# Optimization experiments

Hardware: AMD Instinct MI355X
Metric: run time of the kernel (lower is better)

## Reference

```python
import jax, jax.numpy as jnp
import numpy as np

DIM = 256
HEADS = 8
DIM_HEAD = 64
EPS = 1e-12  # F.normalize eps


def rms_norm(x, w, dim):
    # F.normalize over channel dim (axis=1) * weight * sqrt(dim)
    n = jnp.sqrt(jnp.sum(x * x, axis=1, keepdims=True))
    xn = x / jnp.maximum(n, EPS)
    return xn * w[None, :, None, None] * (dim ** 0.5)


def setup_inputs() -> dict:
    key = jax.random.key(0)
    ks = jax.random.split(key, 4)
    hd = HEADS * DIM_HEAD
    return {
        "x": jax.random.normal(ks[0], (16, DIM, 64, 64), dtype=jnp.float32),
        "norm_w": jnp.ones((DIM,), jnp.float32),
        "qkv_w": jax.random.normal(ks[1], (3 * hd, DIM), jnp.float32) * (DIM ** -0.5),
        "out_w": jax.random.normal(ks[2], (DIM, hd), jnp.float32) * (hd ** -0.5),
        "out_b": jnp.zeros((DIM,), jnp.float32),
        "out_norm_w": jnp.ones((DIM,), jnp.float32),
    }


def reference(x, norm_w, qkv_w, out_w, out_b, out_norm_w):
    b, c, H, W = x.shape
    n = H * W
    scale = DIM_HEAD ** -0.5

    xn = rms_norm(x, norm_w, DIM)
    # 1x1 conv == channel matmul: [3hd, c] x [b, c, H, W]
    qkv = jnp.einsum('oc,bchw->bohw', qkv_w, xn)
    q, k, v = jnp.split(qkv, 3, axis=1)

    def to_heads(t):
        # b (h d) x y -> b h d n
        return t.reshape(b, HEADS, DIM_HEAD, n)

    q = jax.nn.softmax(to_heads(q), axis=2) * scale  # softmax over feature dim d
    k = jax.nn.softmax(to_heads(k), axis=3)          # softmax over spatial n
    v = to_heads(v)

    ctx = jnp.einsum('bhdn,bhen->bhde', k, v)   # [b,h,d,e]
    out = jnp.einsum('bhde,bhdn->bhen', ctx, q) # [b,h,e,n]
    out = out.reshape(b, HEADS * DIM_HEAD, H, W)

    out = jnp.einsum('oc,bchw->bohw', out_w, out) + out_b[None, :, None, None]
    return rms_norm(out, out_norm_w, DIM)
```

## Files before the change

kernel.cpp:

```cpp
#include <hip/hip_runtime.h>

#define C_ 256
#define N_ 4096
#define NH_ 8

typedef unsigned short u16;
typedef unsigned int u32;
typedef __attribute__((ext_vector_type(8))) short s8v;
typedef __attribute__((ext_vector_type(4))) float f4v;

#define MFMA16 __builtin_amdgcn_mfma_f32_16x16x32_bf16

__device__ __forceinline__ float bf2f(u16 b){ union{u32 u; float f;} v; v.u=((u32)b)<<16; return v.f; }
__device__ __forceinline__ u16 f2bf(float f){ union{float f; u32 u;} v; v.f=f; return (u16)((v.u + 0x7FFFu + ((v.u>>16)&1u))>>16); }

__device__ __forceinline__ void gl_lds16(const u16* g, u16* l){
  __builtin_amdgcn_global_load_lds((const __attribute__((address_space(1))) u32*)g,
                                   (__attribute__((address_space(3))) u32*)l, 16, 0, 0);
}

__global__ __launch_bounds__(256) void k_prep(const float* __restrict__ x, const float* __restrict__ nw,
                                              u16* __restrict__ xnT){
  __shared__ float red[256];
  __shared__ float nws[256];
  const int tid = threadIdx.x;
  nws[tid] = nw[tid];
  const int blk = blockIdx.x, b = blk>>6, n0 = (blk&63)*64;
  const int cq = tid>>6, px = tid&63;
  const float* xp = x + (size_t)b*(C_*N_) + (size_t)(cq*64)*N_ + n0 + px;
  float v[64]; float s = 0.f;
  #pragma unroll
  for (int i=0;i<64;i++){ float t = xp[(size_t)i*N_]; v[i]=t; s = fmaf(t,t,s); }
  red[tid] = s;
  __syncthreads();
  const float st = red[px] + red[64+px] + red[128+px] + red[192+px];
  const float r = 16.0f / fmaxf(sqrtf(st), 1e-12f);
  u16* o = xnT + ((size_t)b*4096 + n0 + px)*256 + cq*64;
  #pragma unroll
  for (int i=0;i<64;i+=2){
    *(u32*)(o+i) = (u32)f2bf(v[i]*r*nws[cq*64+i]) | ((u32)f2bf(v[i+1]*r*nws[cq*64+i+1])<<16);
  }
}

__global__ __launch_bounds__(256) void k_wconv(const float* __restrict__ qkvw, const float* __restrict__ ow,
                                               u16* __restrict__ wqkv, u16* __restrict__ owb){
  int i = blockIdx.x*256 + threadIdx.x;
  if (i < 393216) wqkv[i] = f2bf(qkvw[i]);
  else            owb[i-393216] = f2bf(ow[i-393216]);
}

__global__ __launch_bounds__(256,3) void k_kv(const u16* __restrict__ xnT, const u16* __restrict__ wqkv,
    u16* __restrict__ ctxp, float* __restrict__ Mp, float* __restrict__ Sp){
  __shared__ u16 xs[64*256];
  __shared__ u16 pbuf[64*72];
  __shared__ u16 vbuf[64*72];
  const int idx = blockIdx.x;
  const int ch = idx&7, h = (idx>>3)&7, b = idx>>6;
  const int tid=threadIdx.x, w=tid>>6, l=tid&63, l15=l&15, lg=l>>4;
  const int swl = (l15&7)<<4;
  const u16* xb  = xnT + (size_t)b*(4096*256);
  const int srow = (l>>5);
  const int scolB = (l&31)*16;
  s8v ak[8], av[8];
  {
    const u16* wkp = wqkv + (size_t)(512 + h*64 + w*16 + l15)*256 + lg*8;
    #pragma unroll
    for (int cs=0; cs<8; cs++){ ak[cs] = *(const s8v*)(wkp + cs*32); av[cs] = *(const s8v*)(wkp + 131072 + cs*32); }
  }
  int colOff[8];
  #pragma unroll
  for (int cs=0; cs<8; cs++) colOff[cs] = (((cs<<6)+(lg<<4)) ^ swl)>>1;

  f4v acc[4];
  #pragma unroll
  for (int et=0;et<4;et++) acc[et] = (f4v){0.f,0.f,0.f,0.f};
  float ps[4] = {0.f,0.f,0.f,0.f};

  {
    const int n0 = ch*512;
    #pragma unroll
    for (int i=0;i<8;i++){
      int rloc = w*16 + i*2 + srow;
      int scol = scolB ^ ((rloc&7)<<4);
      gl_lds16(xb + (size_t)(n0+rloc)*256 + (scol>>1), &xs[(w*16+i*2)*256]);
    }
  }

  for (int t=0; t<8; ++t){
    __syncthreads();
    f4v kacc[4], vacc[4];
    #pragma unroll
    for (int ns=0;ns<4;ns++){ kacc[ns]=(f4v){0.f,0.f,0.f,0.f}; vacc[ns]=(f4v){0.f,0.f,0.f,0.f}; }
    #pragma unroll
    for (int cs=0; cs<8; cs++){
      #pragma unroll
      for (int ns=0; ns<4; ns++){
        s8v bfr = *(const s8v*)&xs[(ns*16+l15)*256 + colOff[cs]];
        kacc[ns] = MFMA16(ak[cs], bfr, kacc[ns], 0,0,0);
        vacc[ns] = MFMA16(av[cs], bfr, vacc[ns], 0,0,0);
      }
    }
    #pragma unroll
    for (int j=0;j<4;j++){
      const int row = w*16 + lg*4 + j;
      #pragma unroll
      for (int ns=0;ns<4;ns++){
        float e = __expf(kacc[ns][j] - 30.0f);
        ps[j] += e;
        pbuf[row*72 + ns*16+l15] = f2bf(e);
        vbuf[row*72 + ns*16+l15] = f2bf(vacc[ns][j]);
      }
    }
    __syncthreads();
    if (t<7){
      const int n0 = ch*512 + (t+1)*64;
      #pragma unroll
      for (int i=0;i<8;i++){
        int rloc = w*16 + i*2 + srow;
        int scol = scolB ^ ((rloc&7)<<4);
        gl_lds16(xb + (size_t)(n0+rloc)*256 + (scol>>1), &xs[(w*16+i*2)*256]);
      }
    }
    #pragma unroll
    for (int ks=0; ks<2; ks++){
      s8v af = *(const s8v*)(pbuf + (w*16+l15)*72 + ks*32 + lg*8);
      #pragma unroll
      for (int et=0; et<4; et++){
        s8v bv = *(const s8v*)(vbuf + (et*16+l15)*72 + ks*32 + lg*8);
        acc[et] = MFMA16(af, bv, acc[et], 0,0,0);
      }
    }
  }
  u16* cp = ctxp + (((size_t)ch*16 + b)*8 + h)*4096;
  #pragma unroll
  for (int et=0; et<4; et++)
    #pragma unroll
    for (int j=0;j<4;j++)
      cp[(w*16+lg*4+j)*64 + et*16+l15] = f2bf(acc[et][j]);
  #pragma unroll
  for (int j=0;j<4;j++){
    float s = ps[j];
    s += __shfl_xor(s,1); s += __shfl_xor(s,2);
    s += __shfl_xor(s,4); s += __shfl_xor(s,8);
    ps[j] = s;
  }
  if (l15==0){
    #pragma unroll
    for (int j=0;j<4;j++){
      int rg = (b*8+h)*64 + w*16 + lg*4 + j;
      Mp[ch*8192+rg]=30.0f; Sp[ch*8192+rg]=ps[j];
    }
  }
}

__global__ __launch_bounds__(256) void k_comb(const u16* __restrict__ ctxp, const float* __restrict__ Mp,
    const float* __restrict__ Sp, u16* __restrict__ ctxT){
  __shared__ float fs[8][64];
  __shared__ float iSs[64];
  const int bh = blockIdx.x, tid = threadIdx.x;
  if (tid < 64){
    float m[8];
    float Mg = -1e30f;
    #pragma unroll
    for (int ch=0;ch<8;ch++){ m[ch] = Mp[ch*8192 + bh*64 + tid]; Mg = fmaxf(Mg, m[ch]); }
    float Sg = 0.f;
    #pragma unroll
    for (int ch=0;ch<8;ch++){
      float fv = __expf(m[ch]-Mg);
      fs[ch][tid] = fv;
      Sg += Sp[ch*8192 + bh*64 + tid]*fv;
    }
    iSs[tid] = 1.0f / Sg;
  }
  __syncthreads();
  const int e = tid>>2, d0 = (tid&3)*16;
  u16* op = ctxT + (size_t)bh*4096 + e*64 + d0;
  #pragma unroll
  for (int i=0;i<16;i++){
    int d = d0+i;
    float v = 0.f;
    #pragma unroll
    for (int ch=0;ch<8;ch++)
      v += bf2f(ctxp[((size_t)(ch*128)+bh)*4096 + d*64 + e]) * fs[ch][d];
    op[i] = f2bf(v * iSs[d]);
  }
}

__global__ __launch_bounds__(512,2) void k_qout(const u16* __restrict__ xnT, const u16* __restrict__ wqkv,
    const u16* __restrict__ owb, const u16* __restrict__ ctxT,
    const float* __restrict__ ob, const float* __restrict__ onw, float* __restrict__ out){
  __shared__ u16 WQb[2][64*256];
  __shared__ u16 OWb[2][256*64];
  __shared__ u16 qa[8][16*72];
  __shared__ float obs[256], onws[256];
  const int tid = threadIdx.x;
  if (tid < 256){ obs[tid]=ob[tid]; onws[tid]=onw[tid]; }
  const int w=tid>>6, l=tid&63, l15=l&15, lg=l>>4;
  const int swl = (l15&7)<<4;
  const int blk=blockIdx.x, b=blk>>5, n0=(blk&31)*128 + w*16;
  const u16* xb = xnT + ((size_t)b*4096 + n0)*256;
  const u16* cxb0 = ctxT + ((size_t)b*8)*4096;
  u16* qaw = qa[w];
  const int wqRowB = w*8 + (l>>5);
  const int wqColB = (l&31)*16;
  const int owRowB = w*32 + (l>>3);
  const int owColB = (l&7)*16;
  s8v ax[8];
  #pragma unroll
  for (int cs=0;cs<8;cs++) ax[cs] = *(const s8v*)(xb + (size_t)l15*256 + cs*32 + lg*8);
  f4v oacc[16];
  #pragma unroll
  for (int mt=0;mt<16;mt++) oacc[mt] = (f4v){0.f,0.f,0.f,0.f};

  {
    const u16* wqg = wqkv;
    #pragma unroll
    for (int i=0;i<4;i++){
      int row = wqRowB + i*2;
      int scol = wqColB ^ ((row&7)<<4);
      gl_lds16(wqg + (size_t)row*256 + (scol>>1), &WQb[0][(w*8+i*2)*256]);
    }
    #pragma unroll
    for (int i=0;i<4;i++){
      int row = owRowB + i*8;
      int scol = owColB ^ ((row&7)<<4);
      gl_lds16(owb + (size_t)row*512 + 0 + (scol>>1), &OWb[0][(w*32+i*8)*64]);
    }
  }

  for (int h=0; h<8; ++h){
    const int p = h&1;
    asm volatile("s_waitcnt vmcnt(0)" ::: "memory");
    __builtin_amdgcn_s_barrier();
    __builtin_amdgcn_sched_barrier(0);
    s8v bc[8];
    {
      const u16* cxb = cxb0 + (size_t)h*4096;
      #pragma unroll
      for (int ks=0; ks<2; ks++)
        #pragma unroll
        for (int et=0; et<4; et++)
          bc[ks*4+et] = *(const s8v*)(cxb + (et*16+l15)*64 + ks*32 + lg*8);
    }
    if (h<7){
      const u16* wqg = wqkv + (size_t)(h+1)*64*256;
      #pragma unroll
      for (int i=0;i<4;i++){
        int row = wqRowB + i*2;
        int scol = wqColB ^ ((row&7)<<4);
        gl_lds16(wqg + (size_t)row*256 + (scol>>1), &WQb[p^1][(w*8+i*2)*256]);
      }
      #pragma unroll
      for (int i=0;i<4;i++){
        int row = owRowB + i*8;
        int scol = owColB ^ ((row&7)<<4);
        gl_lds16(owb + (size_t)row*512 + (h+1)*64 + (scol>>1), &OWb[p^1][(w*32+i*8)*64]);
      }
    }
    f4v qacc[4];
    #pragma unroll
    for (int dt=0;dt<4;dt++) qacc[dt] = (f4v){0.f,0.f,0.f,0.f};
    #pragma unroll
    for (int dt=0; dt<4; dt++){
      #pragma unroll
      for (int cs=0; cs<8; cs++){
        s8v bw = *(const s8v*)&WQb[p][(dt*16+l15)*256 + ((((cs<<6)+(lg<<4)) ^ swl)>>1)];
        qacc[dt] = MFMA16(ax[cs], bw, qacc[dt], 0,0,0);
      }
    }
    #pragma unroll
    for (int j=0;j<4;j++){
      float m = fmaxf(fmaxf(qacc[0][j],qacc[1][j]),fmaxf(qacc[2][j],qacc[3][j]));
      #pragma unroll
      for (int d=1; d<16; d<<=1) m = fmaxf(m, __shfl_xor(m, d));
      float s = 0.f;
      #pragma unroll
      for (int dt=0;dt<4;dt++){ float e=__expf(qacc[dt][j]-m); qacc[dt][j]=e; s+=e; }
      #pragma unroll
      for (int d=1; d<16; d<<=1) s += __shfl_xor(s, d);
      float inv = 0.125f/s;
      #pragma unroll
      for (int dt=0;dt<4;dt++) qaw[(lg*4+j)*72 + dt*16+l15] = f2bf(qacc[dt][j]*inv);
    }
    f4v aacc[4];
    #pragma unroll
    for (int et=0;et<4;et++) aacc[et] = (f4v){0.f,0.f,0.f,0.f};
    #pragma unroll
    for (int ks=0; ks<2; ks++){
      s8v aq = *(const s8v*)&qaw[l15*72 + ks*32 + lg*8];
      #pragma unroll
      for (int et=0; et<4; et++)
        aacc[et] = MFMA16(aq, bc[ks*4+et], aacc[et], 0,0,0);
    }
    #pragma unroll
    for (int et=0;et<4;et++)
      #pragma unroll
      for (int j=0;j<4;j++)
        qaw[(lg*4+j)*72 + et*16+l15] = f2bf(aacc[et][j]);
    #pragma unroll
    for (int ks=0; ks<2; ks++){
      s8v ba = *(const s8v*)&qaw[l15*72 + ks*32 + lg*8];
      #pragma unroll
      for (int mt=0; mt<16; mt++){
        s8v aw = *(const s8v*)&OWb[p][(mt*16+l15)*64 + ((((ks<<6)+(lg<<4)) ^ swl)>>1)];
        oacc[mt] = MFMA16(aw, ba, oacc[mt], 0,0,0);
      }
    }
  }
  float ss = 0.f;
  #pragma unroll
  for (int mt=0;mt<16;mt++)
    #pragma unroll
    for (int j=0;j<4;j++){
      float v = oacc[mt][j] + obs[mt*16+lg*4+j];
      oacc[mt][j] = v;
      ss = fmaf(v,v,ss);
    }
  ss += __shfl_xor(ss, 16);
  ss += __shfl_xor(ss, 32);
  const float r = 16.0f / fmaxf(sqrtf(ss), 1e-12f);
  float* op = out + (size_t)b*(256*4096) + n0 + l15;
  #pragma unroll
  for (int mt=0;mt<16;mt++)
    #pragma unroll
    for (int j=0;j<4;j++){
      int cout = mt*16+lg*4+j;
      op[(size_t)cout*4096] = oacc[mt][j] * r * onws[cout];
    }
}

extern "C" void kernel_launch(void* const* d_in, const int* in_sizes, int n_in,
                              void* d_out, int out_size, void* d_ws, size_t ws_size,
                              hipStream_t stream){
  const float* x    = (const float*)d_in[0];
  const float* nw   = (const float*)d_in[1];
  const float* qkvw = (const float*)d_in[2];
  const float* ow   = (const float*)d_in[3];
  const float* ob   = (const float*)d_in[4];
  const float* onw  = (const float*)d_in[5];
  float* out = (float*)d_out;
  char* ws = (char*)d_ws;
  u16*   xnT  = (u16*)(ws);
  u16*   wqkv = (u16*)(ws + 33554432);
  u16*   owb  = (u16*)(ws + 34340864);
  u16*   ctxT = (u16*)(ws + 34603008);
  u16*   ctxp = (u16*)(ws + 35651584);
  float* Mp   = (float*)(ws + 44040192);
  float* Sp   = (float*)(ws + 44302336);
  (void)in_sizes; (void)n_in; (void)out_size; (void)ws_size;

  k_wconv<<<2048, 256, 0, stream>>>(qkvw, ow, wqkv, owb);
  k_prep <<<1024, 256, 0, stream>>>(x, nw, xnT);
  k_kv   <<<1024, 256, 0, stream>>>(xnT, wqkv, ctxp, Mp, Sp);
  k_comb <<<128, 256, 0, stream>>>(ctxp, Mp, Sp, ctxT);
  k_qout <<<512, 512, 0, stream>>>(xnT, wqkv, owb, ctxT, ob, onw, out);
}
```

Before: 173.7 us.

## Single-buffer LDS weights in k_qout to raise occupancy to four blocks per CU

The double-buffered LDS tiles for the Q and output-projection weight slices become single buffers, and the per-warp q scratch uses a compact XOR-swizzled layout with no padding. This cuts LDS per block so launch bounds can request four blocks per CU instead of two. To keep single buffers correct, the next head's output weights are loaded after the barrier and the next Q weights after a second mid-iteration barrier. Bias and norm weights are read straight from global memory as float4 instead of being staged in LDS. The cost is an extra barrier per head and less overlap between weight loads and compute, and the higher occupancy target squeezes the register budget, which may cause spills.

```diff
diff --git a/kernel.cpp b/kernel.cpp
--- a/kernel.cpp
+++ b/kernel.cpp
@@ -186,24 +186,21 @@
   }
 }
 
-__global__ __launch_bounds__(512,2) void k_qout(const u16* __restrict__ xnT, const u16* __restrict__ wqkv,
+__global__ __launch_bounds__(512,4) void k_qout(const u16* __restrict__ xnT, const u16* __restrict__ wqkv,
     const u16* __restrict__ owb, const u16* __restrict__ ctxT,
     const float* __restrict__ ob, const float* __restrict__ onw, float* __restrict__ out){
-  __shared__ u16 WQb[2][64*256];
-  __shared__ u16 OWb[2][256*64];
-  __shared__ u16 qa[8][16*72];
-  __shared__ float obs[256], onws[256];
+  __shared__ u16 WQ[64*256];
+  __shared__ u16 OWs[256*64];
+  __shared__ u16 qa[8][1024];
   const int tid = threadIdx.x;
-  if (tid < 256){ obs[tid]=ob[tid]; onws[tid]=onw[tid]; }
   const int w=tid>>6, l=tid&63, l15=l&15, lg=l>>4;
-  const int swl = (l15&7)<<4;
   const int blk=blockIdx.x, b=blk>>5, n0=(blk&31)*128 + w*16;
   const u16* xb = xnT + ((size_t)b*4096 + n0)*256;
   const u16* cxb0 = ctxT + ((size_t)b*8)*4096;
   u16* qaw = qa[w];
-  const int wqRowB = w*8 + (l>>5);
+  const int wqRow0 = (l>>5);
   const int wqColB = (l&31)*16;
-  const int owRowB = w*32 + (l>>3);
+  const int owRow0 = (l>>3);
   const int owColB = (l&7)*16;
   s8v ax[8];
   #pragma unroll
@@ -212,24 +209,20 @@
   #pragma unroll
   for (int mt=0;mt<16;mt++) oacc[mt] = (f4v){0.f,0.f,0.f,0.f};
 
-  {
-    const u16* wqg = wqkv;
-    #pragma unroll
-    for (int i=0;i<4;i++){
-      int row = wqRowB + i*2;
-      int scol = wqColB ^ ((row&7)<<4);
-      gl_lds16(wqg + (size_t)row*256 + (scol>>1), &WQb[0][(w*8+i*2)*256]);
-    }
-    #pragma unroll
-    for (int i=0;i<4;i++){
-      int row = owRowB + i*8;
-      int scol = owColB ^ ((row&7)<<4);
-      gl_lds16(owb + (size_t)row*512 + 0 + (scol>>1), &OWb[0][(w*32+i*8)*64]);
-    }
+  #pragma unroll
+  for (int i=0;i<4;i++){
+    int row = (i*8+w)*2 + wqRow0;
+    int scol = wqColB ^ ((row&15)<<4);
+    gl_lds16(wqkv + (size_t)row*256 + (scol>>1), &WQ[(i*8+w)*512]);
+  }
+  #pragma unroll
+  for (int i=0;i<4;i++){
+    int row = (i*8+w)*8 + owRow0;
+    int scol = owColB ^ ((row&7)<<4);
+    gl_lds16(owb + (size_t)row*512 + (scol>>1), &OWs[(i*8+w)*512]);
   }
 
   for (int h=0; h<8; ++h){
-    const int p = h&1;
     asm volatile("s_waitcnt vmcnt(0)" ::: "memory");
     __builtin_amdgcn_s_barrier();
     __builtin_amdgcn_sched_barrier(0);
@@ -242,91 +235,107 @@
         for (int et=0; et<4; et++)
           bc[ks*4+et] = *(const s8v*)(cxb + (et*16+l15)*64 + ks*32 + lg*8);
     }
+    if (h>0){
+      #pragma unroll
+      for (int i=0;i<4;i++){
+        int row = (i*8+w)*8 + owRow0;
+        int scol = owColB ^ ((row&7)<<4);
+        gl_lds16(owb + (size_t)row*512 + h*64 + (scol>>1), &OWs[(i*8+w)*512]);
+      }
+    }
+    __builtin_amdgcn_sched_barrier(0);
+    f4v qacc[4];
+    #pragma unroll
+    for (int dt=0;dt<4;dt++) qacc[dt] = (f4v){0.f,0.f,0.f,0.f};
+    #pragma unroll
+    for (int dt=0; dt<4; dt++){
+      #pragma unroll
+      for (int cs=0; cs<8; cs++){
+        s8v bw = *(const s8v*)&WQ[(dt*16+l15)*256 + ((((cs<<6)|(lg<<4)) ^ (l15<<4))>>1)];
+        qacc[dt] = MFMA16(ax[cs], bw, qacc[dt], 0,0,0);
+      }
+    }
+    #pragma unroll
+    for (int j=0;j<4;j++){
+      float m = fmaxf(fmaxf(qacc[0][j],qacc[1][j]),fmaxf(qacc[2][j],qacc[3][j]));
+      #pragma unroll
+      for (int d=1; d<16; d<<=1) m = fmaxf(m, __shfl_xor(m, d));
+      float s = 0.f;
+      #pragma unroll
+      for (int dt=0;dt<4;dt++){ float e=__expf(qacc[dt][j]-m); qacc[dt][j]=e; s+=e; }
+      #pragma unroll
+      for (int d=1; d<16; d<<=1) s += __shfl_xor(s, d);
+      float inv = 0.125f/s;
+      #pragma unroll
+      for (int dt=0;dt<4;dt++){
+        int row = lg*4+j;
+        qaw[((row<<6) + dt*16 + l15) ^ ((row&7)<<3)] = f2bf(qacc[dt][j]*inv);
+      }
+    }
+    f4v aacc[4];
+    #pragma unroll
+    for (int et=0;et<4;et++) aacc[et] = (f4v){0.f,0.f,0.f,0.f};
+    #pragma unroll
+    for (int ks=0; ks<2; ks++){
+      s8v aq = *(const s8v*)&qaw[(l15<<6) + ((((ks<<6)|(lg<<4)) ^ ((l15&7)<<4))>>1)];
+      #pragma unroll
+      for (int et=0; et<4; et++)
+        aacc[et] = MFMA16(aq, bc[ks*4+et], aacc[et], 0,0,0);
+    }
+    #pragma unroll
+    for (int et=0;et<4;et++)
+      #pragma unroll
+      for (int j=0;j<4;j++){
+        int row = lg*4+j;
+        qaw[((row<<6) + et*16 + l15) ^ ((row&7)<<3)] = f2bf(aacc[et][j]);
+      }
+    asm volatile("s_waitcnt vmcnt(0)" ::: "memory");
+    __builtin_amdgcn_s_barrier();
+    __builtin_amdgcn_sched_barrier(0);
     if (h<7){
       const u16* wqg = wqkv + (size_t)(h+1)*64*256;
       #pragma unroll
       for (int i=0;i<4;i++){
-        int row = wqRowB + i*2;
-        int scol = wqColB ^ ((row&7)<<4);
-        gl_lds16(wqg + (size_t)row*256 + (scol>>1), &WQb[p^1][(w*8+i*2)*256]);
-      }
-      #pragma unroll
-      for (int i=0;i<4;i++){
-        int row = owRowB + i*8;
-        int scol = owColB ^ ((row&7)<<4);
-        gl_lds16(owb + (size_t)row*512 + (h+1)*64 + (scol>>1), &OWb[p^1][(w*32+i*8)*64]);
-      }
-    }
-    f4v qacc[4];
-    #pragma unroll
-    for (int dt=0;dt<4;dt++) qacc[dt] = (f4v){0.f,0.f,0.f,0.f};
-    #pragma unroll
-    for (int dt=0; dt<4; dt++){
-      #pragma unroll
-      for (int cs=0; cs<8; cs++){
-        s8v bw = *(const s8v*)&WQb[p][(dt*16+l15)*256 + ((((cs<<6)+(lg<<4)) ^ swl)>>1)];
-        qacc[dt] = MFMA16(ax[cs], bw, qacc[dt], 0,0,0);
-      }
-    }
-    #pragma unroll
-    for (int j=0;j<4;j++){
-      float m = fmaxf(fmaxf(qacc[0][j],qacc[1][j]),fmaxf(qacc[2][j],qacc[3][j]));
-      #pragma unroll
-      for (int d=1; d<16; d<<=1) m = fmaxf(m, __shfl_xor(m, d));
-      float s = 0.f;
-      #pragma unroll
-      for (int dt=0;dt<4;dt++){ float e=__expf(qacc[dt][j]-m); qacc[dt][j]=e; s+=e; }
-      #pragma unroll
-      for (int d=1; d<16; d<<=1) s += __shfl_xor(s, d);
-      float inv = 0.125f/s;
-      #pragma unroll
-      for (int dt=0;dt<4;dt++) qaw[(lg*4+j)*72 + dt*16+l15] = f2bf(qacc[dt][j]*inv);
-    }
-    f4v aacc[4];
-    #pragma unroll
-    for (int et=0;et<4;et++) aacc[et] = (f4v){0.f,0.f,0.f,0.f};
+        int row = (i*8+w)*2 + wqRow0;
+        int scol = wqColB ^ ((row&15)<<4);
+        gl_lds16(wqg + (size_t)row*256 + (scol>>1), &WQ[(i*8+w)*512]);
+      }
+    }
+    __builtin_amdgcn_sched_barrier(0);
     #pragma unroll
     for (int ks=0; ks<2; ks++){
-      s8v aq = *(const s8v*)&qaw[l15*72 + ks*32 + lg*8];
-      #pragma unroll
-      for (int et=0; et<4; et++)
-        aacc[et] = MFMA16(aq, bc[ks*4+et], aacc[et], 0,0,0);
-    }
-    #pragma unroll
-    for (int et=0;et<4;et++)
-      #pragma unroll
-      for (int j=0;j<4;j++)
-        qaw[(lg*4+j)*72 + et*16+l15] = f2bf(aacc[et][j]);
-    #pragma unroll
-    for (int ks=0; ks<2; ks++){
-      s8v ba = *(const s8v*)&qaw[l15*72 + ks*32 + lg*8];
+      s8v ba = *(const s8v*)&qaw[(l15<<6) + ((((ks<<6)|(lg<<4)) ^ ((l15&7)<<4))>>1)];
       #pragma unroll
       for (int mt=0; mt<16; mt++){
-        s8v aw = *(const s8v*)&OWb[p][(mt*16+l15)*64 + ((((ks<<6)+(lg<<4)) ^ swl)>>1)];
+        s8v aw = *(const s8v*)&OWs[(mt*16+l15)*64 + ((((ks<<6)|(lg<<4)) ^ ((l15&7)<<4))>>1)];
         oacc[mt] = MFMA16(aw, ba, oacc[mt], 0,0,0);
       }
     }
   }
   float ss = 0.f;
   #pragma unroll
-  for (int mt=0;mt<16;mt++)
-    #pragma unroll
-    for (int j=0;j<4;j++){
-      float v = oacc[mt][j] + obs[mt*16+lg*4+j];
+  for (int mt=0;mt<16;mt++){
+    const float4 o4 = *(const float4*)&ob[mt*16 + lg*4];
+    #pragma unroll
+    for (int j=0;j<4;j++){
+      float v = oacc[mt][j] + ((const float*)&o4)[j];
       oacc[mt][j] = v;
       ss = fmaf(v,v,ss);
     }
+  }
   ss += __shfl_xor(ss, 16);
   ss += __shfl_xor(ss, 32);
   const float r = 16.0f / fmaxf(sqrtf(ss), 1e-12f);
   float* op = out + (size_t)b*(256*4096) + n0 + l15;
   #pragma unroll
-  for (int mt=0;mt<16;mt++)
+  for (int mt=0;mt<16;mt++){
+    const float4 w4 = *(const float4*)&onw[mt*16 + lg*4];
     #pragma unroll
     for (int j=0;j<4;j++){
       int cout = mt*16+lg*4+j;
-      op[(size_t)cout*4096] = oacc[mt][j] * r * onws[cout];
-    }
+      op[(size_t)cout*4096] = oacc[mt][j] * r * ((const float*)&w4)[j];
+    }
+  }
 }
 
 extern "C" void kernel_launch(void* const* d_in, const int* in_sizes, int n_in,
```

New measurement: 328.8 us. +89.3%, slower.
